# Kernel optimization log

Measured on AMD Instinct MI355X. Metric: run time of the kernel, lower is better.

## Reference

```python
import jax, jax.numpy as jnp
import numpy as np

HEADS = 8
DIM_HEAD = 64
CHUNK = 128
EPS = 1e-6
KERNEL_EPS = 1e-4


def softmax_kernel(x, proj, is_query):
    # x: [b,h,n,d], proj: [f,d]  (FAVOR+ positive softmax features)
    d = x.shape[-1]
    data_normalizer = d ** -0.25
    ratio = proj.shape[0] ** -0.5
    data_dash = jnp.einsum('bhnd,fd->bhnf', x * data_normalizer, proj)
    diag = 0.5 * (data_normalizer ** 2) * jnp.sum(x * x, axis=-1, keepdims=True)  # [b,h,n,1]
    if is_query:
        m = jnp.max(data_dash, axis=-1, keepdims=True)
    else:
        m = jnp.max(data_dash, axis=(-1, -2), keepdims=True)
    return ratio * (jnp.exp(data_dash - diag - jax.lax.stop_gradient(m)) + KERNEL_EPS)


def infer_hidden_states(q, k, v, chunk_size=CHUNK):
    # q,k: [b,h,n,f], v: [b,h,n,e]; chunked causal linear attention with carried cumsums
    b, h, n, f = q.shape
    e = v.shape[-1]
    nc = n // chunk_size

    def to_chunks(t):
        return jnp.moveaxis(t.reshape(b, h, nc, chunk_size, t.shape[-1]), 2, 0)

    qs, ks, vs = to_chunks(q), to_chunks(k), to_chunks(v)

    def step(carry, inp):
        Z, S = carry  # [b,h,1,f], [b,h,1,f,e]
        qc, kc, vc = inp
        k_cum = Z + jnp.cumsum(kc, axis=2)                       # [b,h,c,f]
        D_inv = 1.0 / jnp.einsum('bhnf,bhnf->bhn', qc, k_cum + EPS)
        ctx = jnp.einsum('bhnf,bhne->bhnfe', kc, vc)             # [b,h,c,f,e]
        ctx_cum = S + jnp.cumsum(ctx, axis=2)
        out = jnp.einsum('bhnfe,bhnf,bhn->bhne', ctx_cum, qc, D_inv)
        return (k_cum[:, :, -1:], ctx_cum[:, :, -1:]), out

    init = (jnp.zeros((b, h, 1, f), q.dtype), jnp.zeros((b, h, 1, f, e), q.dtype))
    (Z, S), outs = jax.lax.scan(step, init, (qs, ks, vs))
    out = jnp.moveaxis(outs, 0, 2).reshape(b, h, n, e)
    return out, Z[:, :, 0], S[:, :, 0]


def reference(x, proj, Wq, Wk, Wv, Wo, bo):
    b, n, dim = x.shape
    h, dh = HEADS, DIM_HEAD

    def split_heads(t):
        return jnp.transpose(t.reshape(b, n, h, dh), (0, 2, 1, 3))

    q = split_heads(x @ Wq)
    k = split_heads(x @ Wk)
    v = split_heads(x @ Wv)

    qf = softmax_kernel(q, proj, is_query=True)
    kf = softmax_kernel(k, proj, is_query=False)

    out, Z, S = infer_hidden_states(qf, kf, v)
    out = jnp.transpose(out, (0, 2, 1, 3)).reshape(b, n, h * dh)
    out = out @ Wo + bo
    return out, Z, S


def setup_inputs() -> dict:
    key = jax.random.key(0)
    ks = jax.random.split(key, 6)
    b, n, dim = 2, 2048, 512
    f = 256
    return {
        'x': jax.random.normal(ks[0], (b, n, dim), jnp.float32),
        'proj': jax.random.normal(ks[1], (f, DIM_HEAD), jnp.float32),
        'Wq': jax.random.normal(ks[2], (dim, dim), jnp.float32) * (dim ** -0.5),
        'Wk': jax.random.normal(ks[3], (dim, dim), jnp.float32) * (dim ** -0.5),
        'Wv': jax.random.normal(ks[4], (dim, dim), jnp.float32) * (dim ** -0.5),
        'Wo': jax.random.normal(ks[5], (dim, dim), jnp.float32) * (dim ** -0.5),
        'bo': jnp.zeros((dim,), jnp.float32),
    }
```

## Files before the change

### kernel.cpp

```cpp
#include <hip/hip_runtime.h>
#include <hip/hip_bf16.h>
#include <math.h>

#define NB    2
#define NSEQ  2048
#define DIMM  512
#define NH    8
#define DHd   64
#define FF    256
#define CHK   128
#define NCHK  16
#define NBH   16

typedef unsigned short ushort_t;
typedef __attribute__((ext_vector_type(8))) __bf16 bf16x8;
typedef __attribute__((ext_vector_type(4))) float floatx4;

__device__ __forceinline__ unsigned short f2bf(float x) {
    union { __hip_bfloat16 h; unsigned short u; } v;
    v.h = __float2bfloat16(x);
    return v.u;
}
__device__ __forceinline__ float bf2f(unsigned short u) {
    union { unsigned short u2[2]; float f; } v;
    v.u2[0] = 0; v.u2[1] = u;
    return v.f;
}
__device__ __forceinline__ unsigned enc_f(float x) {
    unsigned u = __float_as_uint(x);
    return (u & 0x80000000u) ? ~u : (u | 0x80000000u);
}
__device__ __forceinline__ float dec_f(unsigned e) {
    unsigned u = (e & 0x80000000u) ? (e & 0x7fffffffu) : ~e;
    return __uint_as_float(u);
}

__device__ __forceinline__ void gload16(const void* g, void* l) {
    __builtin_amdgcn_global_load_lds(
        (const __attribute__((address_space(1))) void*)g,
        (__attribute__((address_space(3))) void*)l, 16, 0, 0);
}

__device__ __forceinline__ bf16x8 frag8(const ushort_t* lds, int row, int kb) {
    return *((const bf16x8*)lds + row * 8 + (kb ^ (row & 7)));
}
__device__ __forceinline__ bf16x8 fragS(const ushort_t* lds, int row, int kb) {
    return *((const bf16x8*)lds + row * 16 + (kb ^ (row & 15)));
}

__global__ __launch_bounds__(256)
void prep(const float* __restrict__ x, const float* __restrict__ proj,
          const float* __restrict__ W0, const float* __restrict__ W1,
          const float* __restrict__ W2, const float* __restrict__ W3,
          ushort_t* __restrict__ xb, ushort_t* __restrict__ projb,
          ushort_t* __restrict__ T0, ushort_t* __restrict__ T1,
          ushort_t* __restrict__ T2, ushort_t* __restrict__ T3,
          unsigned* __restrict__ mk_u)
{
    __shared__ float t[32][33];
    const int b = blockIdx.x, tid = threadIdx.x;
    if (b < 2048) {
        const int gid = b * 256 + tid;
        const float4 v = *(const float4*)(x + (size_t)gid * 4);
        union { ushort4 v4; unsigned short s[4]; } pk;
        pk.s[0] = f2bf(v.x); pk.s[1] = f2bf(v.y); pk.s[2] = f2bf(v.z); pk.s[3] = f2bf(v.w);
        ((ushort4*)xb)[gid] = pk.v4;
    } else if (b < 2064) {
        const int gid = (b - 2048) * 256 + tid;
        const float dn = 0.35355339059327379f;
        const float4 v = *(const float4*)(proj + (size_t)gid * 4);
        union { ushort4 v4; unsigned short s[4]; } pk;
        pk.s[0] = f2bf(v.x * dn); pk.s[1] = f2bf(v.y * dn);
        pk.s[2] = f2bf(v.z * dn); pk.s[3] = f2bf(v.w * dn);
        ((ushort4*)projb)[gid] = pk.v4;
    } else if (b < 3088) {
        const int idx = b - 2064;
        const int z = idx >> 8, rem = idx & 255;
        const int bx = rem & 15, by = rem >> 4;
        const float* W = (z == 0) ? W0 : (z == 1) ? W1 : (z == 2) ? W2 : W3;
        ushort_t* T = (z == 0) ? T0 : (z == 1) ? T1 : (z == 2) ? T2 : T3;
        const int x0 = bx * 32, y0 = by * 32;
        const int tx = tid & 31, ty = tid >> 5;
#pragma unroll
        for (int i = 0; i < 4; i++)
            t[ty + i * 8][tx] = W[(size_t)(y0 + ty + i * 8) * DIMM + x0 + tx];
        __syncthreads();
#pragma unroll
        for (int i = 0; i < 4; i++)
            T[(size_t)(x0 + ty + i * 8) * DIMM + y0 + tx] = f2bf(t[tx][ty + i * 8]);
    } else {
        if (tid < NBH) mk_u[tid] = 0u;
    }
}

__device__ __forceinline__ void mfma_mainloop(
    const ushort_t* __restrict__ AG, const ushort_t* __restrict__ BG,
    ushort_t* As, ushort_t* Bs, int ldA, int ldB, int K,
    floatx4 acc[4][4], int tid)
{
    const int lane = tid & 63, wid = tid >> 6;
    const int q = lane >> 4, c = lane & 15;
    const int wm = (wid >> 1) * 64, wn = (wid & 1) * 64;

    for (int k0 = 0; k0 < K; k0 += 64) {
#pragma unroll
        for (int t = 0; t < 4; t++) {
            const int g = t * 256 + tid, r = g >> 3, kb = (g & 7) ^ (r & 7);
            gload16(AG + (size_t)r * ldA + k0 + kb * 8, As + (size_t)g * 8);
        }
#pragma unroll
        for (int t = 0; t < 4; t++) {
            const int g = t * 256 + tid, r = g >> 3, kb = (g & 7) ^ (r & 7);
            gload16(BG + (size_t)r * ldB + k0 + kb * 8, Bs + (size_t)g * 8);
        }
        __syncthreads();
#pragma unroll
        for (int ks = 0; ks < 2; ks++) {
            bf16x8 af[4], bfr[4];
#pragma unroll
            for (int i = 0; i < 4; i++) {
                af[i]  = frag8(As, wm + i * 16 + c, ks * 4 + q);
                bfr[i] = frag8(Bs, wn + i * 16 + c, ks * 4 + q);
            }
#pragma unroll
            for (int i = 0; i < 4; i++)
#pragma unroll
                for (int j = 0; j < 4; j++)
                    acc[i][j] = __builtin_amdgcn_mfma_f32_16x16x32_bf16(
                        af[i], bfr[j], acc[i][j], 0, 0, 0);
        }
        __syncthreads();
    }
}

__global__ __launch_bounds__(256)
void gemm_qkv(const ushort_t* __restrict__ xb,
              const ushort_t* __restrict__ Wtq, const ushort_t* __restrict__ Wtk,
              const ushort_t* __restrict__ Wtv, const ushort_t* __restrict__ projb,
              ushort_t* __restrict__ qb, ushort_t* __restrict__ kb,
              ushort_t* __restrict__ vTb, unsigned* __restrict__ mk_u)
{
    __shared__ alignas(16) ushort_t SM[25600];
    __shared__ float red[256];
    ushort_t* As = SM;
    ushort_t* Bs = SM + 8192;
    ushort_t* PS = SM + 17408;
    const int tid = threadIdx.x;
    const int n0 = blockIdx.x * 128, m0 = blockIdx.y * 128, z = blockIdx.z;
    const ushort_t* Bt = (z == 0) ? Wtq : ((z == 1) ? Wtk : Wtv);

    floatx4 zero = {0.f, 0.f, 0.f, 0.f};
    floatx4 acc[4][4];
#pragma unroll
    for (int i = 0; i < 4; i++)
#pragma unroll
        for (int j = 0; j < 4; j++) acc[i][j] = zero;

    mfma_mainloop(xb + (size_t)m0 * DIMM, Bt + (size_t)n0 * DIMM, As, Bs,
                  DIMM, DIMM, DIMM, acc, tid);

    const int lane = tid & 63, wid = tid >> 6;
    const int q = lane >> 4, cl = lane & 15;
    const int wm = (wid >> 1) * 64, wn = (wid & 1) * 64;

#pragma unroll
    for (int i = 0; i < 4; i++)
#pragma unroll
        for (int j = 0; j < 4; j++) {
            const int col = wn + j * 16 + cl;
#pragma unroll
            for (int r = 0; r < 4; r++) {
                const int row = wm + i * 16 + q * 4 + r;
                SM[row * 136 + col] = f2bf(acc[i][j][r]);
            }
        }
    __syncthreads();

    if (z < 2) {
        ushort_t* ob = (z == 0) ? qb : kb;
        if (z == 1) {
#pragma unroll
            for (int t = 0; t < 4; t++) {
                const int g = t * 256 + tid, f = g >> 3, kbg = (g & 7) ^ (f & 7);
                gload16(projb + (size_t)f * 64 + kbg * 8, PS + (size_t)g * 8);
            }
        }
#pragma unroll
        for (int p = 0; p < 16; p++) {
            const int idx = p * 256 + tid;
            const int row = idx >> 5, c4 = idx & 31;
            ushort4 o = *(const ushort4*)&SM[row * 136 + c4 * 4];
            *(ushort4*)(ob + (size_t)(m0 + row) * DIMM + n0 + c4 * 4) = o;
        }
        if (z == 1) {
            const int bb = m0 >> 11;
            const int h0 = n0 >> 6;
            float mx[2] = {-3.0e38f, -3.0e38f};
#pragma unroll
            for (int half = 0; half < 2; half++) {
                __syncthreads();
#pragma unroll
                for (int hh = 0; hh < 2; hh++) {
                    floatx4 a2[4][4];
#pragma unroll
                    for (int i = 0; i < 4; i++)
#pragma unroll
                        for (int j = 0; j < 4; j++) a2[i][j] = zero;
#pragma unroll
                    for (int ks = 0; ks < 2; ks++) {
                        bf16x8 af[4], bfr[4];
#pragma unroll
                        for (int i = 0; i < 4; i++)
                            af[i] = *(const bf16x8*)&SM[(wm + i * 16 + cl) * 136 + hh * 64 + (ks * 4 + q) * 8];
#pragma unroll
                        for (int j = 0; j < 4; j++)
                            bfr[j] = frag8(PS, wn + j * 16 + cl, ks * 4 + q);
#pragma unroll
                        for (int i = 0; i < 4; i++)
#pragma unroll
                            for (int j = 0; j < 4; j++)
                                a2[i][j] = __builtin_amdgcn_mfma_f32_16x16x32_bf16(
                                    af[i], bfr[j], a2[i][j], 0, 0, 0);
                    }
#pragma unroll
                    for (int i = 0; i < 4; i++)
#pragma unroll
                        for (int j = 0; j < 4; j++)
#pragma unroll
                            for (int r = 0; r < 4; r++) mx[hh] = fmaxf(mx[hh], a2[i][j][r]);
                }
                if (half == 0) {
                    __syncthreads();
#pragma unroll
                    for (int t = 0; t < 4; t++) {
                        const int g = t * 256 + tid, f = g >> 3, kbg = (g & 7) ^ (f & 7);
                        gload16(projb + (size_t)(128 + f) * 64 + kbg * 8, PS + (size_t)g * 8);
                    }
                }
            }
#pragma unroll
            for (int hh = 0; hh < 2; hh++) {
                __syncthreads();
                red[tid] = mx[hh];
                __syncthreads();
                for (int s = 128; s > 0; s >>= 1) {
                    if (tid < s) red[tid] = fmaxf(red[tid], red[tid + s]);
                    __syncthreads();
                }
                if (tid == 0) atomicMax(&mk_u[bb * NH + h0 + hh], enc_f(red[0]));
            }
        }
    } else {
        const int bb = m0 >> 11, nbase = m0 & 2047;
#pragma unroll
        for (int p = 0; p < 16; p++) {
            const int idx = p * 256 + tid;
            const int cl2 = idx >> 5, n4 = idx & 31;
            const int C = n0 + cl2;
            const int h = C >> 6, e = C & 63;
            union { ushort4 v4; unsigned short s[4]; } pk;
#pragma unroll
            for (int k = 0; k < 4; k++) pk.s[k] = SM[(n4 * 4 + k) * 136 + cl2];
            *(ushort4*)(vTb + (((size_t)(bb * NH + h) * 64 + e)) * NSEQ + nbase + n4 * 4) = pk.v4;
        }
    }
}

__global__ __launch_bounds__(256)
void gemm_out(const ushort_t* __restrict__ attnb, const ushort_t* __restrict__ Wto,
              float* __restrict__ out, const float* __restrict__ bias)
{
    __shared__ alignas(16) ushort_t As[8192];
    __shared__ alignas(16) ushort_t Bs[8192];
    const int tid = threadIdx.x;
    const int n0 = blockIdx.x * 128, m0 = blockIdx.y * 128;

    floatx4 zero = {0.f, 0.f, 0.f, 0.f};
    floatx4 acc[4][4];
#pragma unroll
    for (int i = 0; i < 4; i++)
#pragma unroll
        for (int j = 0; j < 4; j++) acc[i][j] = zero;

    mfma_mainloop(attnb + (size_t)m0 * DIMM, Wto + (size_t)n0 * DIMM, As, Bs,
                  DIMM, DIMM, DIMM, acc, tid);

    const int lane = tid & 63, wid = tid >> 6;
    const int q = lane >> 4, c = lane & 15;
    const int wm = (wid >> 1) * 64, wn = (wid & 1) * 64;
#pragma unroll
    for (int i = 0; i < 4; i++)
#pragma unroll
        for (int j = 0; j < 4; j++) {
            const int col = n0 + wn + j * 16 + c;
            const float bv = bias[col];
#pragma unroll
            for (int r = 0; r < 4; r++) {
                const int row = m0 + wm + i * 16 + q * 4 + r;
                out[(size_t)row * DIMM + col] = acc[i][j][r] + bv;
            }
        }
}

__global__ __launch_bounds__(256)
void featx(const ushort_t* __restrict__ qb_, const ushort_t* __restrict__ kb_,
           const ushort_t* __restrict__ projb, const unsigned* __restrict__ mk_u,
           const ushort_t* __restrict__ vTb,
           ushort_t* __restrict__ qfb, ushort_t* __restrict__ kfb,
           float* __restrict__ CTXT, float* __restrict__ Ksum)
{
    __shared__ alignas(16) ushort_t SM[24576];
    __shared__ float dtmp[256];
    __shared__ float diag_l[128];
    __shared__ float mx2[2][128];
    __shared__ float colp[2][256];
    ushort_t* As = SM;
    ushort_t* Bs = SM + 8192;
    const int tid = threadIdx.x, lane = tid & 63, wid = tid >> 6;
    const int q = lane >> 4, cl = lane & 15;
    const int m0 = blockIdx.x * 128, h = blockIdx.y, src = blockIdx.z;
    const int bb = m0 >> 11, nloc = m0 & 2047;
    const int bh = bb * NH + h;
    const int cidx = nloc >> 7;
    const ushort_t* Aq = (src ? kb_ : qb_) + (size_t)m0 * DIMM + h * 64;

    {
        const int row = tid >> 1, half = tid & 1;
        float s = 0.f;
        const ushort_t* p = Aq + (size_t)row * DIMM + half * 32;
#pragma unroll
        for (int d = 0; d < 32; d += 4) {
            ushort4 w = *(const ushort4*)(p + d);
            float a = bf2f(w.x), b2 = bf2f(w.y), c2 = bf2f(w.z), d2 = bf2f(w.w);
            s += a * a + b2 * b2 + c2 * c2 + d2 * d2;
        }
        dtmp[tid] = s;
    }
    __syncthreads();
    if (tid < 128) diag_l[tid] = (dtmp[2 * tid] + dtmp[2 * tid + 1]) * 0.0625f;

#pragma unroll
    for (int t = 0; t < 4; t++) {
        const int g = t * 256 + tid, r = g >> 3, kb = (g & 7) ^ (r & 7);
        gload16(Aq + (size_t)r * DIMM + kb * 8, As + (size_t)g * 8);
    }
#pragma unroll
    for (int t = 0; t < 8; t++) {
        const int g = t * 256 + tid, r = g >> 3, kb = (g & 7) ^ (r & 7);
        gload16(projb + (size_t)r * 64 + kb * 8, Bs + (size_t)g * 8);
    }
    __syncthreads();

    floatx4 zero = {0.f, 0.f, 0.f, 0.f};
    floatx4 acc[4][8];
#pragma unroll
    for (int i = 0; i < 4; i++)
#pragma unroll
        for (int j = 0; j < 8; j++) acc[i][j] = zero;
    const int wm = (wid >> 1) * 64, wn = (wid & 1) * 128;
#pragma unroll
    for (int ks = 0; ks < 2; ks++) {
        bf16x8 af[4], bfr[8];
#pragma unroll
        for (int i = 0; i < 4; i++) af[i] = frag8(As, wm + i * 16 + cl, ks * 4 + q);
#pragma unroll
        for (int j = 0; j < 8; j++) bfr[j] = frag8(Bs, wn + j * 16 + cl, ks * 4 + q);
#pragma unroll
        for (int i = 0; i < 4; i++)
#pragma unroll
            for (int j = 0; j < 8; j++)
                acc[i][j] = __builtin_amdgcn_mfma_f32_16x16x32_bf16(
                    af[i], bfr[j], acc[i][j], 0, 0, 0);
    }

    const float mk = src ? dec_f(mk_u[bh]) : 0.f;
    if (src == 0) {
#pragma unroll
        for (int i = 0; i < 4; i++)
#pragma unroll
            for (int r = 0; r < 4; r++) {
                const int row = wm + i * 16 + q * 4 + r;
                float mx = -3.0e38f;
#pragma unroll
                for (int j = 0; j < 8; j++) mx = fmaxf(mx, acc[i][j][r]);
                mx = fmaxf(mx, __shfl_xor(mx, 1)); mx = fmaxf(mx, __shfl_xor(mx, 2));
                mx = fmaxf(mx, __shfl_xor(mx, 4)); mx = fmaxf(mx, __shfl_xor(mx, 8));
                if (cl == 0) mx2[wid & 1][row] = mx;
            }
    }
    __syncthreads();

#pragma unroll
    for (int i = 0; i < 4; i++)
#pragma unroll
        for (int r = 0; r < 4; r++) {
            const int row = wm + i * 16 + q * 4 + r;
            const float cc = diag_l[row] + (src ? mk : fmaxf(mx2[0][row], mx2[1][row]));
#pragma unroll
            for (int j = 0; j < 8; j++)
                acc[i][j][r] = 0.0625f * (__expf(acc[i][j][r] - cc) + 1.0e-4f);
        }

    if (src) {
#pragma unroll
        for (int j = 0; j < 8; j++) {
            float s = 0.f;
#pragma unroll
            for (int i = 0; i < 4; i++)
                s += acc[i][j][0] + acc[i][j][1] + acc[i][j][2] + acc[i][j][3];
            s += __shfl_xor(s, 16);
            s += __shfl_xor(s, 32);
            if (q == 0) colp[wid >> 1][wn + j * 16 + cl] = s;
        }
    }

    ushort_t* ff = src ? kfb : qfb;
    const size_t frow = (size_t)bh * NSEQ + nloc;

#pragma unroll
    for (int hf = 0; hf < 2; hf++) {
        __syncthreads();
        if ((wid & 1) == hf) {
#pragma unroll
            for (int i = 0; i < 4; i++)
#pragma unroll
                for (int j = 0; j < 8; j++) {
                    const int col = j * 16 + cl;
#pragma unroll
                    for (int r = 0; r < 4; r++) {
                        const int row = wm + i * 16 + q * 4 + r;
                        SM[row * 132 + col] = f2bf(acc[i][j][r]);
                    }
                }
        }
        if (hf == 0 && src) {
            Ksum[((size_t)bh * NCHK + cidx) * FF + tid] = colp[0][tid] + colp[1][tid];
        }
        __syncthreads();
#pragma unroll
        for (int p = 0; p < 16; p++) {
            const int idx = p * 256 + tid;
            const int row = idx >> 5, c4 = idx & 31;
            ushort4 o = *(const ushort4*)&SM[row * 132 + c4 * 4];
            *(ushort4*)(ff + (frow + row) * FF + hf * 128 + c4 * 4) = o;
        }
    }

    if (src == 0) return;

    __syncthreads();
    ushort_t* Vs = SM;
    ushort_t* T  = SM + 8192;
    const ushort_t* Vg = vTb + ((size_t)bh * 64) * NSEQ + nloc;
#pragma unroll
    for (int t = 0; t < 4; t++) {
        const int g = t * 256 + tid, r = g >> 4, kb = (g & 15) ^ (r & 15);
        gload16(Vg + (size_t)r * NSEQ + kb * 8, Vs + (size_t)g * 8);
    }

    const size_t cbase = ((size_t)bh * NCHK + cidx) * 64;
#pragma unroll
    for (int fq = 0; fq < 4; fq++) {
        if ((wid & 1) == (fq >> 1)) {
#pragma unroll
            for (int jj = 0; jj < 4; jj++) {
                const int j = (fq & 1) * 4 + jj;
#pragma unroll
                for (int i = 0; i < 4; i++)
#pragma unroll
                    for (int r = 0; r < 4; r++) {
                        const int n = wm + i * 16 + q * 4 + r;
                        T[(jj * 16 + cl) * 136 + n] = f2bf(acc[i][j][r]);
                    }
            }
        }
        __syncthreads();
        floatx4 accc[4];
#pragma unroll
        for (int jj = 0; jj < 4; jj++) accc[jj] = zero;
#pragma unroll
        for (int kt = 0; kt < 4; kt++) {
            const bf16x8 av = fragS(Vs, wid * 16 + cl, kt * 4 + q);
#pragma unroll
            for (int jj = 0; jj < 4; jj++) {
                const bf16x8 bv = *(const bf16x8*)(T + (jj * 16 + cl) * 136 + (kt * 4 + q) * 8);
                accc[jj] = __builtin_amdgcn_mfma_f32_16x16x32_bf16(av, bv, accc[jj], 0, 0, 0);
            }
        }
#pragma unroll
        for (int jj = 0; jj < 4; jj++) {
            const int f = fq * 64 + jj * 16 + cl;
#pragma unroll
            for (int r = 0; r < 4; r++) {
                const int e = wid * 16 + q * 4 + r;
                CTXT[(cbase + e) * FF + f] = accc[jj][r];
            }
        }
        __syncthreads();
    }
}

__global__ void prefix_zs(float* __restrict__ Ksum, float* __restrict__ Zout,
                          const float* __restrict__ CTXT, ushort_t* __restrict__ ctxp,
                          float* __restrict__ Sout)
{
    const int b = blockIdx.x;
    if (b < 1024) {
        const int idx = b * 256 + threadIdx.x;
        const int bh = idx >> 14, ef = idx & 16383;
        const int e = ef >> 8, f = ef & 255;
        float run = 0.f;
#pragma unroll
        for (int c = 0; c < NCHK; c++) {
            const size_t o = (((size_t)bh * NCHK + c) * 64 + e) * FF + f;
            const float t = CTXT[o];
            ctxp[o] = f2bf(run);
            run += t;
        }
        Sout[((size_t)bh * FF + f) * 64 + e] = run;
    } else {
        const int idx = (b - 1024) * 256 + threadIdx.x;
        const int bh = idx >> 8, f = idx & 255;
        float run = 0.f;
#pragma unroll
        for (int c = 0; c < NCHK; c++) {
            const size_t o = ((size_t)(bh * NCHK + c)) * FF + f;
            const float t = Ksum[o];
            Ksum[o] = run;
            run += t;
        }
        Zout[(size_t)bh * FF + f] = run;
    }
}

__global__ __launch_bounds__(256)
void chunk_out_mfma(const ushort_t* __restrict__ qfb, const ushort_t* __restrict__ kfb,
                    const ushort_t* __restrict__ vTb, const float* __restrict__ Zex,
                    const ushort_t* __restrict__ ctxp, ushort_t* __restrict__ attnb)
{
    __shared__ alignas(16) ushort_t Sld[16384];
    __shared__ alignas(16) ushort_t As[8192];
    __shared__ alignas(16) ushort_t Bs[8192];
    __shared__ float zeps[256];
    __shared__ float rows_part[2][128];
    __shared__ float denp[256];
    __shared__ float den_l[128];

    const int tid = threadIdx.x, lane = tid & 63, wid = tid >> 6;
    const int q = lane >> 4, cl = lane & 15;
    const int bh = blockIdx.x >> 4, c = blockIdx.x & 15;
    const int bb = bh >> 3, h = bh & 7;
    const int n0 = c * CHK;
    const ushort_t* Q  = qfb + ((size_t)bh * NSEQ + n0) * FF;
    const ushort_t* Kf = kfb + ((size_t)bh * NSEQ + n0) * FF;

    zeps[tid] = Zex[((size_t)bh * NCHK + c) * FF + tid] + 1.0e-6f;

    floatx4 zero = {0.f, 0.f, 0.f, 0.f};
    floatx4 acc1[4][4];
#pragma unroll
    for (int i = 0; i < 4; i++)
#pragma unroll
        for (int j = 0; j < 4; j++) acc1[i][j] = zero;
    const int wm = (wid >> 1) * 64, wn = (wid & 1) * 64;
    for (int k0 = 0; k0 < FF; k0 += 64) {
#pragma unroll
        for (int t = 0; t < 4; t++) {
            const int g = t * 256 + tid, r = g >> 3, kb = (g & 7) ^ (r & 7);
            gload16(Q + (size_t)r * FF + k0 + kb * 8, As + (size_t)g * 8);
        }
#pragma unroll
        for (int t = 0; t < 4; t++) {
            const int g = t * 256 + tid, r = g >> 3, kb = (g & 7) ^ (r & 7);
            gload16(Kf + (size_t)r * FF + k0 + kb * 8, Bs + (size_t)g * 8);
        }
        __syncthreads();
#pragma unroll
        for (int ks = 0; ks < 2; ks++) {
            bf16x8 af[4], bfr[4];
#pragma unroll
            for (int i = 0; i < 4; i++) {
                af[i]  = frag8(As, wm + i * 16 + cl, ks * 4 + q);
                bfr[i] = frag8(Bs, wn + i * 16 + cl, ks * 4 + q);
            }
#pragma unroll
            for (int i = 0; i < 4; i++)
#pragma unroll
                for (int j = 0; j < 4; j++)
                    acc1[i][j] = __builtin_amdgcn_mfma_f32_16x16x32_bf16(
                        af[i], bfr[j], acc1[i][j], 0, 0, 0);
        }
        __syncthreads();
    }
#pragma unroll
    for (int i = 0; i < 4; i++)
#pragma unroll
        for (int r = 0; r < 4; r++) {
            const int row = wm + i * 16 + q * 4 + r;
            float part = 0.f;
#pragma unroll
            for (int j = 0; j < 4; j++) {
                const int col = wn + j * 16 + cl;
                const float v = (col <= row) ? acc1[i][j][r] : 0.f;
                part += v;
                Sld[(row * 16 + ((col >> 3) ^ (row & 15))) * 8 + (col & 7)] = f2bf(v);
            }
            part += __shfl_xor(part, 1); part += __shfl_xor(part, 2);
            part += __shfl_xor(part, 4); part += __shfl_xor(part, 8);
            if (cl == 0) rows_part[wid & 1][row] = part;
        }
    __syncthreads();

    floatx4 acc2[4][2];
#pragma unroll
    for (int i = 0; i < 4; i++)
#pragma unroll
        for (int j = 0; j < 2; j++) acc2[i][j] = zero;
    const ushort_t* Vt = vTb + ((size_t)bh * 64) * NSEQ + n0;
    for (int k0 = 0; k0 < CHK; k0 += 64) {
#pragma unroll
        for (int t = 0; t < 2; t++) {
            const int g = t * 256 + tid, r = g >> 3, kb = (g & 7) ^ (r & 7);
            gload16(Vt + (size_t)r * NSEQ + k0 + kb * 8, As + (size_t)g * 8);
        }
        __syncthreads();
#pragma unroll
        for (int ks = 0; ks < 2; ks++) {
            bf16x8 af[4], bfr[2];
            const int kbS = (k0 >> 3) + ks * 4 + q;
#pragma unroll
            for (int i = 0; i < 4; i++) af[i] = frag8(As, i * 16 + cl, ks * 4 + q);
#pragma unroll
            for (int j = 0; j < 2; j++) bfr[j] = fragS(Sld, wid * 32 + j * 16 + cl, kbS);
#pragma unroll
            for (int i = 0; i < 4; i++)
#pragma unroll
                for (int j = 0; j < 2; j++)
                    acc2[i][j] = __builtin_amdgcn_mfma_f32_16x16x32_bf16(
                        af[i], bfr[j], acc2[i][j], 0, 0, 0);
        }
        __syncthreads();
    }

    const ushort_t* Cp = ctxp + ((size_t)bh * NCHK + c) * 64 * FF;
    float dacc = 0.f;
    const int drow = tid & 127, dhalf = tid >> 7;
    for (int k0 = 0; k0 < FF; k0 += 64) {
#pragma unroll
        for (int t = 0; t < 2; t++) {
            const int g = t * 256 + tid, r = g >> 3, kb = (g & 7) ^ (r & 7);
            gload16(Cp + (size_t)r * FF + k0 + kb * 8, As + (size_t)g * 8);
        }
#pragma unroll
        for (int t = 0; t < 4; t++) {
            const int g = t * 256 + tid, r = g >> 3, kb = (g & 7) ^ (r & 7);
            gload16(Q + (size_t)r * FF + k0 + kb * 8, Bs + (size_t)g * 8);
        }
        __syncthreads();
#pragma unroll
        for (int ks = 0; ks < 2; ks++) {
            bf16x8 af[4], bfr[2];
#pragma unroll
            for (int i = 0; i < 4; i++) af[i] = frag8(As, i * 16 + cl, ks * 4 + q);
#pragma unroll
            for (int j = 0; j < 2; j++) bfr[j] = frag8(Bs, wid * 32 + j * 16 + cl, ks * 4 + q);
#pragma unroll
            for (int i = 0; i < 4; i++)
#pragma unroll
                for (int j = 0; j < 2; j++)
                    acc2[i][j] = __builtin_amdgcn_mfma_f32_16x16x32_bf16(
                        af[i], bfr[j], acc2[i][j], 0, 0, 0);
        }
#pragma unroll
        for (int gi = 0; gi < 4; gi++) {
            const int kb = dhalf * 4 + gi;
            const ushort_t* gp = Bs + ((size_t)drow * 8 + (kb ^ (drow & 7))) * 8;
            const int kbase = k0 + kb * 8;
#pragma unroll
            for (int e2 = 0; e2 < 8; e2++)
                dacc = fmaf(bf2f(gp[e2]), zeps[kbase + e2], dacc);
        }
        __syncthreads();
    }
    denp[tid] = dacc;
    __syncthreads();
    if (tid < 128)
        den_l[tid] = rows_part[0][tid] + rows_part[1][tid] + denp[tid] + denp[tid + 128];
    __syncthreads();

#pragma unroll
    for (int j = 0; j < 2; j++) {
        const int row = wid * 32 + j * 16 + cl;
        const float dinv = 1.0f / den_l[row];
#pragma unroll
        for (int i = 0; i < 4; i++)
#pragma unroll
            for (int r = 0; r < 4; r++) {
                const int e = i * 16 + q * 4 + r;
                Sld[row * 68 + e] = f2bf(acc2[i][j][r] * dinv);
            }
    }
    __syncthreads();
#pragma unroll
    for (int p = 0; p < 8; p++) {
        const int idx = p * 256 + tid;
        const int row = idx >> 4, e4 = idx & 15;
        ushort4 o = *(const ushort4*)&Sld[row * 68 + e4 * 4];
        *(ushort4*)(attnb + ((size_t)(bb * NSEQ + n0 + row)) * DIMM + h * 64 + e4 * 4) = o;
    }
}

extern "C" void kernel_launch(void* const* d_in, const int* in_sizes, int n_in,
                              void* d_out, int out_size, void* d_ws, size_t ws_size,
                              hipStream_t stream)
{
    (void)in_sizes; (void)n_in; (void)out_size; (void)ws_size;
    const float* x    = (const float*)d_in[0];
    const float* proj = (const float*)d_in[1];
    const float* Wq   = (const float*)d_in[2];
    const float* Wk   = (const float*)d_in[3];
    const float* Wv   = (const float*)d_in[4];
    const float* Wo   = (const float*)d_in[5];
    const float* bo   = (const float*)d_in[6];
    float* out = (float*)d_out;

    char* W = (char*)d_ws;
    float*    CTXT = (float*)W;              W += (size_t)16777216;
    ushort_t* qfb  = (ushort_t*)W;           W += (size_t)16777216;
    ushort_t* kfb  = (ushort_t*)W;           W += (size_t)16777216;
    ushort_t* qb   = (ushort_t*)W;           W += (size_t)4194304;
    ushort_t* kb   = (ushort_t*)W;           W += (size_t)4194304;
    ushort_t* xb   = (ushort_t*)W;           W += (size_t)4194304;
    ushort_t* vTb  = (ushort_t*)W;           W += (size_t)4194304;
    ushort_t* Wtq  = (ushort_t*)W;           W += (size_t)524288;
    ushort_t* Wtk  = (ushort_t*)W;           W += (size_t)524288;
    ushort_t* Wtv  = (ushort_t*)W;           W += (size_t)524288;
    ushort_t* Wto  = (ushort_t*)W;           W += (size_t)524288;
    ushort_t* projb = (ushort_t*)W;          W += (size_t)32768;
    float*    Ksum = (float*)W;              W += (size_t)262144;
    unsigned* mk_u = (unsigned*)W;           W += (size_t)256;

    ushort_t* ctxp = qb;
    ushort_t* attnb = xb;

    float* Zout = out + (size_t)4096 * 512;
    float* Sout = Zout + (size_t)NBH * FF;

    hipLaunchKernelGGL(prep, dim3(3089), dim3(256), 0, stream,
                       x, proj, Wq, Wk, Wv, Wo, xb, projb, Wtq, Wtk, Wtv, Wto, mk_u);
    hipLaunchKernelGGL(gemm_qkv, dim3(4, 32, 3), dim3(256), 0, stream,
                       xb, Wtq, Wtk, Wtv, projb, qb, kb, vTb, mk_u);
    hipLaunchKernelGGL(featx, dim3(32, 8, 2), dim3(256), 0, stream,
                       qb, kb, projb, mk_u, vTb, qfb, kfb, CTXT, Ksum);
    hipLaunchKernelGGL(prefix_zs, dim3(1040), dim3(256), 0, stream,
                       Ksum, Zout, CTXT, ctxp, Sout);
    hipLaunchKernelGGL(chunk_out_mfma, dim3(256), dim3(256), 0, stream,
                       qfb, kfb, vTb, Ksum, ctxp, attnb);
    hipLaunchKernelGGL(gemm_out, dim3(4, 32), dim3(256), 0, stream, attnb, Wto, out, bo);
}
```

Before: 155.6 us.

## Fuse query feature map computation into chunk output kernel, keep qf in LDS

Query FAVOR+ features are no longer computed in the feature kernel and written to global memory. Instead, the chunk output kernel projects q against proj with MFMA, applies the row-max exponent, and stores the bf16 features in a swizzled LDS buffer that both the intra-chunk and inter-chunk GEMMs read. This removes a 16 MB global write and repeated reads of qf. In exchange the chunk kernel uses much more shared memory (a new 64 KB QF buffer), which may lower occupancy, and ctxp gets its own workspace buffer because qb is still needed.

Measured after the change: 149.6 us, median of 2. 1.04x faster.

```diff
diff --git a/kernel.cpp b/kernel.cpp
--- a/kernel.cpp
+++ b/kernel.cpp
@@ -303,26 +303,24 @@
 }
 
 __global__ __launch_bounds__(256)
-void featx(const ushort_t* __restrict__ qb_, const ushort_t* __restrict__ kb_,
-           const ushort_t* __restrict__ projb, const unsigned* __restrict__ mk_u,
-           const ushort_t* __restrict__ vTb,
-           ushort_t* __restrict__ qfb, ushort_t* __restrict__ kfb,
-           float* __restrict__ CTXT, float* __restrict__ Ksum)
+void featk(const ushort_t* __restrict__ kb_, const ushort_t* __restrict__ projb,
+           const unsigned* __restrict__ mk_u, const ushort_t* __restrict__ vTb,
+           ushort_t* __restrict__ kfb, float* __restrict__ CTXT,
+           float* __restrict__ Ksum)
 {
     __shared__ alignas(16) ushort_t SM[24576];
     __shared__ float dtmp[256];
     __shared__ float diag_l[128];
-    __shared__ float mx2[2][128];
     __shared__ float colp[2][256];
     ushort_t* As = SM;
     ushort_t* Bs = SM + 8192;
     const int tid = threadIdx.x, lane = tid & 63, wid = tid >> 6;
     const int q = lane >> 4, cl = lane & 15;
-    const int m0 = blockIdx.x * 128, h = blockIdx.y, src = blockIdx.z;
+    const int m0 = blockIdx.x * 128, h = blockIdx.y;
     const int bb = m0 >> 11, nloc = m0 & 2047;
     const int bh = bb * NH + h;
     const int cidx = nloc >> 7;
-    const ushort_t* Aq = (src ? kb_ : qb_) + (size_t)m0 * DIMM + h * 64;
+    const ushort_t* Aq = kb_ + (size_t)m0 * DIMM + h * 64;
 
     {
         const int row = tid >> 1, half = tid & 1;
@@ -372,51 +370,32 @@
                 acc[i][j] = __builtin_amdgcn_mfma_f32_16x16x32_bf16(
                     af[i], bfr[j], acc[i][j], 0, 0, 0);
     }
-
-    const float mk = src ? dec_f(mk_u[bh]) : 0.f;
-    if (src == 0) {
-#pragma unroll
-        for (int i = 0; i < 4; i++)
-#pragma unroll
-            for (int r = 0; r < 4; r++) {
-                const int row = wm + i * 16 + q * 4 + r;
-                float mx = -3.0e38f;
-#pragma unroll
-                for (int j = 0; j < 8; j++) mx = fmaxf(mx, acc[i][j][r]);
-                mx = fmaxf(mx, __shfl_xor(mx, 1)); mx = fmaxf(mx, __shfl_xor(mx, 2));
-                mx = fmaxf(mx, __shfl_xor(mx, 4)); mx = fmaxf(mx, __shfl_xor(mx, 8));
-                if (cl == 0) mx2[wid & 1][row] = mx;
-            }
-    }
-    __syncthreads();
-
+    __syncthreads();
+
+    const float mk = dec_f(mk_u[bh]);
 #pragma unroll
     for (int i = 0; i < 4; i++)
 #pragma unroll
         for (int r = 0; r < 4; r++) {
             const int row = wm + i * 16 + q * 4 + r;
-            const float cc = diag_l[row] + (src ? mk : fmaxf(mx2[0][row], mx2[1][row]));
+            const float cc = diag_l[row] + mk;
 #pragma unroll
             for (int j = 0; j < 8; j++)
                 acc[i][j][r] = 0.0625f * (__expf(acc[i][j][r] - cc) + 1.0e-4f);
         }
 
-    if (src) {
-#pragma unroll
-        for (int j = 0; j < 8; j++) {
-            float s = 0.f;
-#pragma unroll
-            for (int i = 0; i < 4; i++)
-                s += acc[i][j][0] + acc[i][j][1] + acc[i][j][2] + acc[i][j][3];
-            s += __shfl_xor(s, 16);
-            s += __shfl_xor(s, 32);
-            if (q == 0) colp[wid >> 1][wn + j * 16 + cl] = s;
-        }
-    }
-
-    ushort_t* ff = src ? kfb : qfb;
+#pragma unroll
+    for (int j = 0; j < 8; j++) {
+        float s = 0.f;
+#pragma unroll
+        for (int i = 0; i < 4; i++)
+            s += acc[i][j][0] + acc[i][j][1] + acc[i][j][2] + acc[i][j][3];
+        s += __shfl_xor(s, 16);
+        s += __shfl_xor(s, 32);
+        if (q == 0) colp[wid >> 1][wn + j * 16 + cl] = s;
+    }
+
     const size_t frow = (size_t)bh * NSEQ + nloc;
-
 #pragma unroll
     for (int hf = 0; hf < 2; hf++) {
         __syncthreads();
@@ -433,7 +412,7 @@
                     }
                 }
         }
-        if (hf == 0 && src) {
+        if (hf == 0) {
             Ksum[((size_t)bh * NCHK + cidx) * FF + tid] = colp[0][tid] + colp[1][tid];
         }
         __syncthreads();
@@ -442,11 +421,9 @@
             const int idx = p * 256 + tid;
             const int row = idx >> 5, c4 = idx & 31;
             ushort4 o = *(const ushort4*)&SM[row * 132 + c4 * 4];
-            *(ushort4*)(ff + (frow + row) * FF + hf * 128 + c4 * 4) = o;
-        }
-    }
-
-    if (src == 0) return;
+            *(ushort4*)(kfb + (frow + row) * FF + hf * 128 + c4 * 4) = o;
+        }
+    }
 
     __syncthreads();
     ushort_t* Vs = SM;
@@ -534,10 +511,12 @@
 }
 
 __global__ __launch_bounds__(256)
-void chunk_out_mfma(const ushort_t* __restrict__ qfb, const ushort_t* __restrict__ kfb,
-                    const ushort_t* __restrict__ vTb, const float* __restrict__ Zex,
-                    const ushort_t* __restrict__ ctxp, ushort_t* __restrict__ attnb)
+void chunk_out_mfma(const ushort_t* __restrict__ qb_, const ushort_t* __restrict__ projb,
+                    const ushort_t* __restrict__ kfb, const ushort_t* __restrict__ vTb,
+                    const float* __restrict__ Zex, const ushort_t* __restrict__ ctxp,
+                    ushort_t* __restrict__ attnb)
 {
+    __shared__ alignas(16) ushort_t QF[32768];
     __shared__ alignas(16) ushort_t Sld[16384];
     __shared__ alignas(16) ushort_t As[8192];
     __shared__ alignas(16) ushort_t Bs[8192];
@@ -545,18 +524,99 @@
     __shared__ float rows_part[2][128];
     __shared__ float denp[256];
     __shared__ float den_l[128];
+    __shared__ float dtmp[256];
+    __shared__ float diag_l[128];
+    __shared__ float mx2[2][128];
 
     const int tid = threadIdx.x, lane = tid & 63, wid = tid >> 6;
     const int q = lane >> 4, cl = lane & 15;
     const int bh = blockIdx.x >> 4, c = blockIdx.x & 15;
     const int bb = bh >> 3, h = bh & 7;
     const int n0 = c * CHK;
-    const ushort_t* Q  = qfb + ((size_t)bh * NSEQ + n0) * FF;
     const ushort_t* Kf = kfb + ((size_t)bh * NSEQ + n0) * FF;
+    const ushort_t* Aq = qb_ + ((size_t)(bb * NSEQ + n0)) * DIMM + h * 64;
 
     zeps[tid] = Zex[((size_t)bh * NCHK + c) * FF + tid] + 1.0e-6f;
 
+    {
+        const int row = tid >> 1, half = tid & 1;
+        float s = 0.f;
+        const ushort_t* p = Aq + (size_t)row * DIMM + half * 32;
+#pragma unroll
+        for (int d = 0; d < 32; d += 4) {
+            ushort4 w = *(const ushort4*)(p + d);
+            float a = bf2f(w.x), b2 = bf2f(w.y), c2 = bf2f(w.z), d2 = bf2f(w.w);
+            s += a * a + b2 * b2 + c2 * c2 + d2 * d2;
+        }
+        dtmp[tid] = s;
+    }
+    __syncthreads();
+    if (tid < 128) diag_l[tid] = (dtmp[2 * tid] + dtmp[2 * tid + 1]) * 0.0625f;
+
+#pragma unroll
+    for (int t = 0; t < 4; t++) {
+        const int g = t * 256 + tid, r = g >> 3, kb = (g & 7) ^ (r & 7);
+        gload16(Aq + (size_t)r * DIMM + kb * 8, As + (size_t)g * 8);
+    }
+#pragma unroll
+    for (int t = 0; t < 8; t++) {
+        const int g = t * 256 + tid, r = g >> 3, kb = (g & 7) ^ (r & 7);
+        gload16(projb + (size_t)r * 64 + kb * 8, Sld + (size_t)g * 8);
+    }
+    __syncthreads();
+
     floatx4 zero = {0.f, 0.f, 0.f, 0.f};
+    {
+        floatx4 accq[4][8];
+#pragma unroll
+        for (int i = 0; i < 4; i++)
+#pragma unroll
+            for (int j = 0; j < 8; j++) accq[i][j] = zero;
+        const int wmF = (wid >> 1) * 64, wnF = (wid & 1) * 128;
+#pragma unroll
+        for (int ks = 0; ks < 2; ks++) {
+            bf16x8 af[4], bfr[8];
+#pragma unroll
+            for (int i = 0; i < 4; i++) af[i] = frag8(As, wmF + i * 16 + cl, ks * 4 + q);
+#pragma unroll
+            for (int j = 0; j < 8; j++) bfr[j] = frag8(Sld, wnF + j * 16 + cl, ks * 4 + q);
+#pragma unroll
+            for (int i = 0; i < 4; i++)
+#pragma unroll
+                for (int j = 0; j < 8; j++)
+                    accq[i][j] = __builtin_amdgcn_mfma_f32_16x16x32_bf16(
+                        af[i], bfr[j], accq[i][j], 0, 0, 0);
+        }
+#pragma unroll
+        for (int i = 0; i < 4; i++)
+#pragma unroll
+            for (int r = 0; r < 4; r++) {
+                const int row = wmF + i * 16 + q * 4 + r;
+                float mx = -3.0e38f;
+#pragma unroll
+                for (int j = 0; j < 8; j++) mx = fmaxf(mx, accq[i][j][r]);
+                mx = fmaxf(mx, __shfl_xor(mx, 1)); mx = fmaxf(mx, __shfl_xor(mx, 2));
+                mx = fmaxf(mx, __shfl_xor(mx, 4)); mx = fmaxf(mx, __shfl_xor(mx, 8));
+                if (cl == 0) mx2[wid & 1][row] = mx;
+            }
+        __syncthreads();
+#pragma unroll
+        for (int i = 0; i < 4; i++)
+#pragma unroll
+            for (int r = 0; r < 4; r++) {
+                const int row = wmF + i * 16 + q * 4 + r;
+                const float cc = diag_l[row] + fmaxf(mx2[0][row], mx2[1][row]);
+#pragma unroll
+                for (int j = 0; j < 8; j++) {
+                    const int col = wnF + j * 16 + cl;
+                    const float v = 0.0625f * (__expf(accq[i][j][r] - cc) + 1.0e-4f);
+                    const int s = col >> 6, fp = col & 63;
+                    QF[s * 8192 + (row * 8 + ((fp >> 3) ^ (row & 7))) * 8 + (fp & 7)] = f2bf(v);
+                }
+            }
+    }
+    __syncthreads();
+
     floatx4 acc1[4][4];
 #pragma unroll
     for (int i = 0; i < 4; i++)
@@ -567,20 +627,16 @@
 #pragma unroll
         for (int t = 0; t < 4; t++) {
             const int g = t * 256 + tid, r = g >> 3, kb = (g & 7) ^ (r & 7);
-            gload16(Q + (size_t)r * FF + k0 + kb * 8, As + (size_t)g * 8);
-        }
-#pragma unroll
-        for (int t = 0; t < 4; t++) {
-            const int g = t * 256 + tid, r = g >> 3, kb = (g & 7) ^ (r & 7);
             gload16(Kf + (size_t)r * FF + k0 + kb * 8, Bs + (size_t)g * 8);
         }
         __syncthreads();
+        const ushort_t* QFs = QF + (k0 >> 6) * 8192;
 #pragma unroll
         for (int ks = 0; ks < 2; ks++) {
             bf16x8 af[4], bfr[4];
 #pragma unroll
             for (int i = 0; i < 4; i++) {
-                af[i]  = frag8(As, wm + i * 16 + cl, ks * 4 + q);
+                af[i]  = frag8(QFs, wm + i * 16 + cl, ks * 4 + q);
                 bfr[i] = frag8(Bs, wn + i * 16 + cl, ks * 4 + q);
             }
 #pragma unroll
@@ -651,19 +707,15 @@
             const int g = t * 256 + tid, r = g >> 3, kb = (g & 7) ^ (r & 7);
             gload16(Cp + (size_t)r * FF + k0 + kb * 8, As + (size_t)g * 8);
         }
-#pragma unroll
-        for (int t = 0; t < 4; t++) {
-            const int g = t * 256 + tid, r = g >> 3, kb = (g & 7) ^ (r & 7);
-            gload16(Q + (size_t)r * FF + k0 + kb * 8, Bs + (size_t)g * 8);
-        }
-        __syncthreads();
+        __syncthreads();
+        const ushort_t* QFs = QF + (k0 >> 6) * 8192;
 #pragma unroll
         for (int ks = 0; ks < 2; ks++) {
             bf16x8 af[4], bfr[2];
 #pragma unroll
             for (int i = 0; i < 4; i++) af[i] = frag8(As, i * 16 + cl, ks * 4 + q);
 #pragma unroll
-            for (int j = 0; j < 2; j++) bfr[j] = frag8(Bs, wid * 32 + j * 16 + cl, ks * 4 + q);
+            for (int j = 0; j < 2; j++) bfr[j] = frag8(QFs, wid * 32 + j * 16 + cl, ks * 4 + q);
 #pragma unroll
             for (int i = 0; i < 4; i++)
 #pragma unroll
@@ -674,7 +726,7 @@
 #pragma unroll
         for (int gi = 0; gi < 4; gi++) {
             const int kb = dhalf * 4 + gi;
-            const ushort_t* gp = Bs + ((size_t)drow * 8 + (kb ^ (drow & 7))) * 8;
+            const ushort_t* gp = QFs + ((size_t)drow * 8 + (kb ^ (drow & 7))) * 8;
             const int kbase = k0 + kb * 8;
 #pragma unroll
             for (int e2 = 0; e2 < 8; e2++)
@@ -726,8 +778,8 @@
 
     char* W = (char*)d_ws;
     float*    CTXT = (float*)W;              W += (size_t)16777216;
-    ushort_t* qfb  = (ushort_t*)W;           W += (size_t)16777216;
     ushort_t* kfb  = (ushort_t*)W;           W += (size_t)16777216;
+    ushort_t* ctxp = (ushort_t*)W;           W += (size_t)8388608;
     ushort_t* qb   = (ushort_t*)W;           W += (size_t)4194304;
     ushort_t* kb   = (ushort_t*)W;           W += (size_t)4194304;
     ushort_t* xb   = (ushort_t*)W;           W += (size_t)4194304;
@@ -740,7 +792,6 @@
     float*    Ksum = (float*)W;              W += (size_t)262144;
     unsigned* mk_u = (unsigned*)W;           W += (size_t)256;
 
-    ushort_t* ctxp = qb;
     ushort_t* attnb = xb;
 
     float* Zout = out + (size_t)4096 * 512;
@@ -750,11 +801,11 @@
                        x, proj, Wq, Wk, Wv, Wo, xb, projb, Wtq, Wtk, Wtv, Wto, mk_u);
     hipLaunchKernelGGL(gemm_qkv, dim3(4, 32, 3), dim3(256), 0, stream,
                        xb, Wtq, Wtk, Wtv, projb, qb, kb, vTb, mk_u);
-    hipLaunchKernelGGL(featx, dim3(32, 8, 2), dim3(256), 0, stream,
-                       qb, kb, projb, mk_u, vTb, qfb, kfb, CTXT, Ksum);
+    hipLaunchKernelGGL(featk, dim3(32, 8), dim3(256), 0, stream,
+                       kb, projb, mk_u, vTb, kfb, CTXT, Ksum);
     hipLaunchKernelGGL(prefix_zs, dim3(1040), dim3(256), 0, stream,
                        Ksum, Zout, CTXT, ctxp, Sout);
     hipLaunchKernelGGL(chunk_out_mfma, dim3(256), dim3(256), 0, stream,
-                       qfb, kfb, vTb, Ksum, ctxp, attnb);
+                       qb, projb, kfb, vTb, Ksum, ctxp, attnb);
     hipLaunchKernelGGL(gemm_out, dim3(4, 32), dim3(256), 0, stream, attnb, Wto, out, bo);
 }
```
